# Performance work log

Measured on AMD Instinct MI355X. Metric: run time of the kernel, lower is better.

The kernel has to match this reference:

```python
import jax, jax.numpy as jnp
import numpy as np

N_S = 50000   # support points
N_Q = 50000   # query points
H = 32        # neighbors per query
K = 15        # kernel points
C_IN = 64
C_OUT = 64
G = 8         # group norm groups
RADIUS = 1.0
SIGMA = 0.6
EPS = 1e-5
NEG_SLOPE = 0.1


def setup_inputs() -> dict:
    key = jax.random.key(0)
    ks = jax.random.split(key, 8)
    s_feats = jax.random.normal(ks[0], (N_S, C_IN), jnp.float32)
    q_points = jax.random.uniform(ks[1], (N_Q, 3), jnp.float32)
    s_points = jax.random.uniform(ks[2], (N_S, 3), jnp.float32)
    # index N_S is the shadow (padding) neighbor
    neighbor_indices = jax.random.randint(ks[3], (N_Q, H), 0, N_S + 1)
    # kernel point dispositions: fixed points inside a ball of RADIUS
    d = jax.random.normal(ks[4], (K, 3), jnp.float32)
    d = d / jnp.linalg.norm(d, axis=1, keepdims=True)
    r = jax.random.uniform(ks[5], (K, 1), jnp.float32) ** (1.0 / 3.0)
    kernel_points = d * r * RADIUS                      # (K,3)
    weights = jax.random.normal(ks[6], (K, C_IN, C_OUT), jnp.float32) * (1.0 / np.sqrt(K * C_IN))
    bias = jax.random.normal(ks[7], (C_OUT,), jnp.float32) * 0.01
    gamma = jnp.ones((C_OUT,), jnp.float32)
    beta = jnp.zeros((C_OUT,), jnp.float32)
    return dict(s_feats=s_feats, q_points=q_points, s_points=s_points,
                neighbor_indices=neighbor_indices, kernel_points=kernel_points,
                weights=weights, bias=bias, gamma=gamma, beta=beta)


def kpconv(s_feats, q_points, s_points, neighbor_indices, kernel_points, weights, bias):
    # pad support set with shadow point (1e10) and zero features
    pad_pts = jnp.concatenate([s_points, jnp.full((1, 3), 1e10, s_points.dtype)], axis=0)
    pad_feats = jnp.concatenate([s_feats, jnp.zeros((1, s_feats.shape[1]), s_feats.dtype)], axis=0)
    nbr_pts = pad_pts[neighbor_indices] - q_points[:, None, :]              # (M,H,3)
    diff = nbr_pts[:, :, None, :] - kernel_points[None, None, :, :]         # (M,H,K,3)
    sq_d = jnp.sum(diff * diff, axis=-1)                                    # (M,H,K)
    # linear correlation influence, clamped at 0
    w = jnp.maximum(1.0 - jnp.sqrt(sq_d) / SIGMA, 0.0)                      # (M,H,K)
    nbr_feats = pad_feats[neighbor_indices]                                 # (M,H,Cin)
    weighted = jnp.einsum('mhk,mhc->mkc', w, nbr_feats)                     # (M,K,Cin)
    out = jnp.einsum('mkc,kcd->md', weighted, weights)                      # (M,Cout)
    # normalize by number of valid neighbors (feature-sum > 0 test, as in KPConv)
    nbr_num = jnp.sum(jnp.sum(nbr_feats, axis=-1) > 0, axis=-1)             # (M,)
    nbr_num = jnp.maximum(nbr_num, 1).astype(out.dtype)
    return out / nbr_num[:, None] + bias


def group_norm(x, gamma, beta):
    # matches GroupNorm wrapper: (M,C) -> (1,C,M) -> nn.GroupNorm -> (M,C)
    M, C = x.shape
    xg = x.T.reshape(G, C // G, M)                                          # (G,Cg,M)
    mean = xg.mean(axis=(1, 2), keepdims=True)
    var = xg.var(axis=(1, 2), keepdims=True)
    xn = ((xg - mean) / jnp.sqrt(var + EPS)).reshape(C, M).T                # (M,C)
    return xn * gamma + beta


def reference(s_feats, q_points, s_points, neighbor_indices, kernel_points, weights, bias, gamma, beta):
    x = kpconv(s_feats, q_points, s_points, neighbor_indices, kernel_points, weights, bias)
    x = group_norm(x, gamma, beta)
    x = jnp.where(x >= 0, x, NEG_SLOPE * x)                                 # LeakyReLU(0.1)
    return x[:, None, :]                                                    # unsqueeze(1): (M,1,Cout)
```

## Files before the change

kernel.cpp:

```cpp
#include <hip/hip_runtime.h>
#include <hip/hip_bf16.h>
#include <math.h>

#define NSUP 50000
#define NQ   50000
#define NH   32
#define NK   15
#define NG   8
#define INV_SIGMA (1.0f/0.6f)
#define GN_EPS 1e-5f
#define NEG  0.1f

#define QB   16
#define NBLK (NQ/QB)

#define OFF_ROWSUM 0
#define OFF_FB     50048
#define OFF_WB     (OFF_FB + 1600000)
#define OFF_PS     (OFF_WB + 30720)
#define OFF_PQ     (OFF_PS + NBLK*8)
#define OFF_STAT   (OFF_PQ + NBLK*8)

typedef __attribute__((ext_vector_type(8))) short bf16x8;
typedef __attribute__((ext_vector_type(4))) float f32x4;
typedef __attribute__((ext_vector_type(4))) unsigned int u32x4;

__device__ __forceinline__ short f2bf(float x) {
    __hip_bfloat16 h = __float2bfloat16(x);
    return *reinterpret_cast<short*>(&h);
}

__global__ __launch_bounds__(256) void k_prep(const float* __restrict__ sf,
                                              float* __restrict__ rowsum,
                                              unsigned short* __restrict__ fb,
                                              const float* __restrict__ wts,
                                              unsigned short* __restrict__ wb) {
    if (blockIdx.x < 12500) {
        int row  = (blockIdx.x * 256 + threadIdx.x) >> 6;
        int lane = threadIdx.x & 63;
        if (row >= NSUP) return;
        float v = sf[(size_t)row * 64 + lane];
        fb[(size_t)row * 64 + lane] = (unsigned short)f2bf(v);
        float s = v;
        #pragma unroll
        for (int o = 32; o; o >>= 1) s += __shfl_down(s, o);
        if (lane == 0) rowsum[row] = s;
    } else {
        int idx = (blockIdx.x - 12500) * 256 + threadIdx.x;
        if (idx >= 30 * 4 * 64 * 8) return;
        int j  = idx & 7;
        int l  = (idx >> 3) & 63;
        int n  = (idx >> 9) & 3;
        int ks = idx >> 11;
        int r  = ks * 32 + ((l >> 4) << 3) + j;
        int d  = n * 16 + (l & 15);
        wb[idx] = (unsigned short)f2bf(wts[(size_t)r * 64 + d]);
    }
}

__global__ __launch_bounds__(256, 5) void k_conv(
    const unsigned short* __restrict__ fb, const float* __restrict__ qpts,
    const float* __restrict__ spts,  const int*   __restrict__ nidx,
    const float* __restrict__ kpts,  const unsigned short* __restrict__ wb,
    const float* __restrict__ bias,  const float* __restrict__ rowsum,
    float* __restrict__ conv_out, float* __restrict__ part_s, float* __restrict__ part_q)
{
    __shared__ __align__(16) short wl16[16 * 968];
    __shared__ __align__(16) float kp4[16][4];
    __shared__ float rcl[16];

    const int tid  = threadIdx.x;
    const int wv   = tid >> 6;
    const int lane = tid & 63;
    const int g    = lane >> 4;
    const int c16  = lane & 15;

    if (tid < 16) {
        if (tid < NK) {
            kp4[tid][0] = kpts[tid*3+0];
            kp4[tid][1] = kpts[tid*3+1];
            kp4[tid][2] = kpts[tid*3+2];
        } else {
            kp4[tid][0] = 1e8f; kp4[tid][1] = 1e8f; kp4[tid][2] = 1e8f;
        }
        kp4[tid][3] = 0.f;
    }
    __syncthreads();

    const float kx = kp4[c16][0], ky = kp4[c16][1], kz = kp4[c16][2];

    const int qbase = blockIdx.x * QB;
    char*  WV  = (char*)wl16 + wv * 7424;
    float* XYP = (float*)WV;
    char*  FP  = WV + 2560;

    f32x4 pacc[4][4];
    #pragma unroll
    for (int a = 0; a < 4; a++)
        #pragma unroll
        for (int b = 0; b < 4; b++) pacc[a][b] = (f32x4){0.f,0.f,0.f,0.f};

    const int h    = lane & 31;
    const int half = lane >> 5;

    #pragma unroll
    for (int pp = 0; pp < 2; pp++) {
        const int qq = pp*2 + half;
        const int m  = qbase + wv*4 + qq;
        const float qx = qpts[m*3+0], qy = qpts[m*3+1], qz = qpts[m*3+2];
        const int  id  = nidx[(size_t)m * NH + h];
        const bool val = (id < NSUP);
        const int  ii  = val ? id : 0;
        const float dx = spts[ii*3+0]-qx, dy = spts[ii*3+1]-qy, dz = spts[ii*3+2]-qz;
        const float rs = rowsum[ii];
        unsigned long long bal = __ballot(val && rs > 0.f);
        int cA = __popcll(bal & 0xffffffffull); if (cA < 1) cA = 1;
        int cB = __popcll(bal >> 32);           if (cB < 1) cB = 1;
        if (lane == 0)  rcl[wv*4 + pp*2]     = 1.0f / (float)cA;
        if (lane == 32) rcl[wv*4 + pp*2 + 1] = 1.0f / (float)cB;
        const int si = (pp*64 + half*32 + h) * 5;
        XYP[si]     = val ? dx : 1e10f;
        XYP[si + 1] = dy;
        XYP[si + 2] = dz;
    }

    const int gr = lane >> 3;
    const int gs = lane & 7;
    int   idA[4], idB[4];
    u32x4 vA[4], vB[4];
    {
        const int m0 = qbase + wv*4;
        #pragma unroll
        for (int i = 0; i < 4; i++) idA[i] = nidx[(size_t)m0*NH + i*8 + gr];
        #pragma unroll
        for (int i = 0; i < 4; i++) {
            const int id2 = (idA[i] < NSUP) ? idA[i] : 0;
            vA[i] = *(const u32x4*)((const char*)fb + (size_t)id2*128 + gs*16);
        }
        const int m1 = qbase + wv*4 + 1;
        #pragma unroll
        for (int i = 0; i < 4; i++) idB[i] = nidx[(size_t)m1*NH + i*8 + gr];
    }

    #pragma unroll
    for (int q = 0; q < 4; q++) {
        const int pp = q >> 1, e = q & 1;
        u32x4* vc  = (q & 1) ? vB  : vA;
        u32x4* vn  = (q & 1) ? vA  : vB;
        int*   idn = (q & 1) ? idA : idB;
        int*   idt = (q & 1) ? idB : idA;

        #pragma unroll
        for (int i = 0; i < 4; i++)
            *(u32x4*)(FP + (i*8 + gr)*144 + ((gs ^ i) << 4)) = vc[i];

        if (q < 3) {
            #pragma unroll
            for (int i = 0; i < 4; i++) {
                const int id2 = (idn[i] < NSUP) ? idn[i] : 0;
                vn[i] = *(const u32x4*)((const char*)fb + (size_t)id2*128 + gs*16);
            }
        }
        if (q < 2) {
            const int mn = qbase + wv*4 + q + 2;
            #pragma unroll
            for (int i = 0; i < 4; i++) idt[i] = nidx[(size_t)mn*NH + i*8 + gr];
        }

        union { unsigned short u[8]; bf16x8 v; } ua;
        #pragma unroll
        for (int j = 0; j < 8; j++) {
            const int xi = (pp*64 + e*32 + g*8 + j) * 5;
            const float px = XYP[xi], py = XYP[xi+1], pz = XYP[xi+2];
            const float ex = px - kx, ey = py - ky, ez = pz - kz;
            const float sq = fmaf(ex, ex, fmaf(ey, ey, ez * ez));
            const float w  = fmaxf(1.0f - sqrtf(sq) * INV_SIGMA, 0.f);
            ua.u[j] = (unsigned short)f2bf(w);
        }

        #pragma unroll
        for (int ct = 0; ct < 4; ct++) {
            const char* vb = FP + (g*8)*144
                           + (((((ct << 1) | (c16 >> 3)) ^ g) & 7) << 4)
                           + ((c16 & 7) << 1);
            union { unsigned short u[8]; bf16x8 v; } ub;
            #pragma unroll
            for (int j = 0; j < 8; j++)
                ub.u[j] = *(const unsigned short*)(vb + j*144);
            pacc[q][ct] = __builtin_amdgcn_mfma_f32_16x16x32_bf16(ua.v, ub.v, pacc[q][ct], 0, 0, 0);
        }
    }

    __syncthreads();

    #pragma unroll
    for (int qq = 0; qq < 4; qq++) {
        #pragma unroll
        for (int ct = 0; ct < 4; ct++) {
            #pragma unroll
            for (int i = 0; i < 4; i++) {
                const int kk = g*4 + i;
                if (kk < NK)
                    wl16[(wv*4 + qq)*968 + kk*64 + ct*16 + c16] = f2bf(pacc[qq][ct][i]);
            }
        }
    }
    __syncthreads();

    f32x4 facc = (f32x4){0.f,0.f,0.f,0.f};
    const int z = lane >> 4;
    const short* ap = wl16 + c16*968 + z*8;
    const unsigned short* bp = wb + ((size_t)(wv * 64 + lane)) * 8;
    #pragma unroll 6
    for (int ks = 0; ks < 30; ks++) {
        bf16x8 a = *(const bf16x8*)(ap + ks*32);
        bf16x8 b = *(const bf16x8*)(bp + (size_t)ks*2048);
        facc = __builtin_amdgcn_mfma_f32_16x16x32_bf16(a, b, facc, 0, 0, 0);
    }

    const int   d  = wv*16 + c16;
    const float bs = bias[d];
    float gl = 0.f, gq = 0.f;
    #pragma unroll
    for (int i = 0; i < 4; i++) {
        const int row = z*4 + i;
        const float y = facc[i] * rcl[row] + bs;
        conv_out[(size_t)(qbase + row)*64 + d] = y;
        gl += y;
        gq = fmaf(y, y, gq);
    }
    #pragma unroll
    for (int msk = 1; msk <= 4; msk <<= 1) { gl += __shfl_xor(gl, msk); gq += __shfl_xor(gq, msk); }
    gl += __shfl_xor(gl, 16); gq += __shfl_xor(gq, 16);
    gl += __shfl_xor(gl, 32); gq += __shfl_xor(gq, 32);
    if ((lane & 55) == 0) {
        const int grp = wv*2 + (lane >> 3);
        part_s[(size_t)blockIdx.x * 8 + grp] = gl;
        part_q[(size_t)blockIdx.x * 8 + grp] = gq;
    }
}

__global__ __launch_bounds__(1024) void k_reduce(const float* __restrict__ part_s,
                                                 const float* __restrict__ part_q,
                                                 float* __restrict__ stat) {
    __shared__ double ds[128][8], dq[128][8];
    const int t = threadIdx.x;
    const int g = t & 7, chunk = t >> 3;
    const int per = (NBLK + 127) / 128;
    double s = 0.0, q = 0.0;
    int lo = chunk * per, hi = lo + per; if (hi > NBLK) hi = NBLK;
    for (int i = lo; i < hi; i++) {
        s += (double)part_s[(size_t)i * 8 + g];
        q += (double)part_q[(size_t)i * 8 + g];
    }
    ds[chunk][g] = s; dq[chunk][g] = q;
    __syncthreads();
    if (t < 8) {
        double S = 0.0, Q = 0.0;
        for (int cix = 0; cix < 128; cix++) { S += ds[cix][t]; Q += dq[cix][t]; }
        const double cnt = (double)(64 / NG) * (double)NQ;
        double mean = S / cnt;
        double var  = Q / cnt - mean * mean;
        stat[t]     = (float)mean;
        stat[8 + t] = (float)(1.0 / sqrt(var + (double)GN_EPS));
    }
}

__global__ __launch_bounds__(256) void k_apply(float* __restrict__ out,
                                               const float* __restrict__ stat,
                                               const float* __restrict__ gamma,
                                               const float* __restrict__ beta) {
    const int n4 = NQ * 64 / 4;
    for (int idx = blockIdx.x * 256 + threadIdx.x; idx < n4; idx += gridDim.x * 256) {
        float4 v = ((const float4*)out)[idx];
        const int c4 = idx & 15;
        const int g  = c4 >> 1;
        const float mean = stat[g], istd = stat[8 + g];
        const float4 ga = ((const float4*)gamma)[c4];
        const float4 be = ((const float4*)beta)[c4];
        float4 r;
        r.x = (v.x - mean) * istd * ga.x + be.x; r.x = r.x >= 0.f ? r.x : NEG * r.x;
        r.y = (v.y - mean) * istd * ga.y + be.y; r.y = r.y >= 0.f ? r.y : NEG * r.y;
        r.z = (v.z - mean) * istd * ga.z + be.z; r.z = r.z >= 0.f ? r.z : NEG * r.z;
        r.w = (v.w - mean) * istd * ga.w + be.w; r.w = r.w >= 0.f ? r.w : NEG * r.w;
        ((float4*)out)[idx] = r;
    }
}

extern "C" void kernel_launch(void* const* d_in, const int* in_sizes, int n_in,
                              void* d_out, int out_size, void* d_ws, size_t ws_size,
                              hipStream_t stream) {
    const float* sfeats = (const float*)d_in[0];
    const float* qpts   = (const float*)d_in[1];
    const float* spts   = (const float*)d_in[2];
    const int*   nidx   = (const int*)  d_in[3];
    const float* kpts   = (const float*)d_in[4];
    const float* wts    = (const float*)d_in[5];
    const float* bias   = (const float*)d_in[6];
    const float* gamma  = (const float*)d_in[7];
    const float* beta   = (const float*)d_in[8];

    float* ws = (float*)d_ws;
    float*          rowsum = ws + OFF_ROWSUM;
    unsigned short* fb     = (unsigned short*)(ws + OFF_FB);
    unsigned short* wb     = (unsigned short*)(ws + OFF_WB);
    float*          ps     = ws + OFF_PS;
    float*          pq     = ws + OFF_PQ;
    float*          stat   = ws + OFF_STAT;
    float*          out    = (float*)d_out;

    k_prep <<<dim3(12740), dim3(256), 0, stream>>>(sfeats, rowsum, fb, wts, wb);
    k_conv <<<dim3(NBLK),  dim3(256), 0, stream>>>(fb, qpts, spts, nidx, kpts,
                                                   wb, bias, rowsum, out, ps, pq);
    k_reduce<<<dim3(1),    dim3(1024), 0, stream>>>(ps, pq, stat);
    k_apply <<<dim3(1024), dim3(256), 0, stream>>>(out, stat, gamma, beta);
}
```

Measured before the change: 77.80 us.

## Split conv block across 8 waves with split-K final GEMM and perm-packed loads

Each k_conv block of 16 queries now runs 512 threads (8 waves) instead of 256. In the first phase each wave handles 2 queries instead of 4. The second GEMM is split along K across two wave halves, and the partial sums are combined through shared memory. The B-operand gather now reads 32-bit words and packs them with v_perm instead of eight 16-bit LDS loads. The XYP stride is also padded to 6 floats so it can use float2 accesses. This raises wave-level parallelism and shortens each wave's serial chain, at the cost of an extra barrier, an LDS reduction and a different occupancy/register budget.

```diff
diff --git a/kernel.cpp b/kernel.cpp
--- a/kernel.cpp
+++ b/kernel.cpp
@@ -58,19 +58,19 @@
     }
 }
 
-__global__ __launch_bounds__(256, 5) void k_conv(
+__global__ __launch_bounds__(512, 4) void k_conv(
     const unsigned short* __restrict__ fb, const float* __restrict__ qpts,
     const float* __restrict__ spts,  const int*   __restrict__ nidx,
     const float* __restrict__ kpts,  const unsigned short* __restrict__ wb,
     const float* __restrict__ bias,  const float* __restrict__ rowsum,
     float* __restrict__ conv_out, float* __restrict__ part_s, float* __restrict__ part_q)
 {
-    __shared__ __align__(16) short wl16[16 * 968];
+    __shared__ __align__(16) char U[49152];
     __shared__ __align__(16) float kp4[16][4];
     __shared__ float rcl[16];
 
     const int tid  = threadIdx.x;
-    const int wv   = tid >> 6;
+    const int w    = tid >> 6;
     const int lane = tid & 63;
     const int g    = lane >> 4;
     const int c16  = lane & 15;
@@ -90,23 +90,15 @@
     const float kx = kp4[c16][0], ky = kp4[c16][1], kz = kp4[c16][2];
 
     const int qbase = blockIdx.x * QB;
-    char*  WV  = (char*)wl16 + wv * 7424;
+    char*  WV  = U + w * 6144;
     float* XYP = (float*)WV;
-    char*  FP  = WV + 2560;
-
-    f32x4 pacc[4][4];
-    #pragma unroll
-    for (int a = 0; a < 4; a++)
-        #pragma unroll
-        for (int b = 0; b < 4; b++) pacc[a][b] = (f32x4){0.f,0.f,0.f,0.f};
+    char*  FP  = WV + 1536;
 
     const int h    = lane & 31;
     const int half = lane >> 5;
 
-    #pragma unroll
-    for (int pp = 0; pp < 2; pp++) {
-        const int qq = pp*2 + half;
-        const int m  = qbase + wv*4 + qq;
+    {
+        const int m  = qbase + w*2 + half;
         const float qx = qpts[m*3+0], qy = qpts[m*3+1], qz = qpts[m*3+2];
         const int  id  = nidx[(size_t)m * NH + h];
         const bool val = (id < NSUP);
@@ -116,11 +108,11 @@
         unsigned long long bal = __ballot(val && rs > 0.f);
         int cA = __popcll(bal & 0xffffffffull); if (cA < 1) cA = 1;
         int cB = __popcll(bal >> 32);           if (cB < 1) cB = 1;
-        if (lane == 0)  rcl[wv*4 + pp*2]     = 1.0f / (float)cA;
-        if (lane == 32) rcl[wv*4 + pp*2 + 1] = 1.0f / (float)cB;
-        const int si = (pp*64 + half*32 + h) * 5;
-        XYP[si]     = val ? dx : 1e10f;
-        XYP[si + 1] = dy;
+        if (lane == 0)  rcl[w*2]     = 1.0f / (float)cA;
+        if (lane == 32) rcl[w*2 + 1] = 1.0f / (float)cB;
+        const int si = (half*32 + h) * 6;
+        float2 xy; xy.x = val ? dx : 1e10f; xy.y = dy;
+        *(float2*)&XYP[si] = xy;
         XYP[si + 2] = dz;
     }
 
@@ -129,114 +121,128 @@
     int   idA[4], idB[4];
     u32x4 vA[4], vB[4];
     {
-        const int m0 = qbase + wv*4;
+        const int m0 = qbase + w*2;
         #pragma unroll
         for (int i = 0; i < 4; i++) idA[i] = nidx[(size_t)m0*NH + i*8 + gr];
+        #pragma unroll
+        for (int i = 0; i < 4; i++) idB[i] = nidx[(size_t)(m0+1)*NH + i*8 + gr];
         #pragma unroll
         for (int i = 0; i < 4; i++) {
             const int id2 = (idA[i] < NSUP) ? idA[i] : 0;
             vA[i] = *(const u32x4*)((const char*)fb + (size_t)id2*128 + gs*16);
         }
-        const int m1 = qbase + wv*4 + 1;
-        #pragma unroll
-        for (int i = 0; i < 4; i++) idB[i] = nidx[(size_t)m1*NH + i*8 + gr];
-    }
-
+    }
+
+    f32x4 pacc[2][4];
     #pragma unroll
-    for (int q = 0; q < 4; q++) {
-        const int pp = q >> 1, e = q & 1;
-        u32x4* vc  = (q & 1) ? vB  : vA;
-        u32x4* vn  = (q & 1) ? vA  : vB;
-        int*   idn = (q & 1) ? idA : idB;
-        int*   idt = (q & 1) ? idB : idA;
+    for (int a = 0; a < 2; a++)
+        #pragma unroll
+        for (int b = 0; b < 4; b++) pacc[a][b] = (f32x4){0.f,0.f,0.f,0.f};
+
+    const unsigned selp = 0x05040100u + ((c16 & 1) ? 0x02020202u : 0u);
+
+    #pragma unroll
+    for (int e = 0; e < 2; e++) {
+        u32x4* vc = e ? vB : vA;
 
         #pragma unroll
         for (int i = 0; i < 4; i++)
             *(u32x4*)(FP + (i*8 + gr)*144 + ((gs ^ i) << 4)) = vc[i];
 
-        if (q < 3) {
+        if (e == 0) {
             #pragma unroll
             for (int i = 0; i < 4; i++) {
-                const int id2 = (idn[i] < NSUP) ? idn[i] : 0;
-                vn[i] = *(const u32x4*)((const char*)fb + (size_t)id2*128 + gs*16);
+                const int id2 = (idB[i] < NSUP) ? idB[i] : 0;
+                vB[i] = *(const u32x4*)((const char*)fb + (size_t)id2*128 + gs*16);
             }
         }
-        if (q < 2) {
-            const int mn = qbase + wv*4 + q + 2;
+
+        union { unsigned short u[8]; bf16x8 v; } ua;
+        #pragma unroll
+        for (int j = 0; j < 8; j++) {
+            const int si = (e*32 + g*8 + j) * 6;
+            const float2 pxy = *(const float2*)&XYP[si];
+            const float  pz  = XYP[si + 2];
+            const float ex = pxy.x - kx, ey = pxy.y - ky, ez = pz - kz;
+            const float sq = fmaf(ex, ex, fmaf(ey, ey, ez * ez));
+            const float wv = fmaxf(1.0f - sqrtf(sq) * INV_SIGMA, 0.f);
+            ua.u[j] = (unsigned short)f2bf(wv);
+        }
+
+        #pragma unroll
+        for (int ct = 0; ct < 4; ct++) {
+            const char* vb = FP + g*1152
+                           + (((((ct << 1) | (c16 >> 3)) ^ g) & 7) << 4)
+                           + ((c16 & 6) << 1);
+            union { unsigned u32[4]; bf16x8 v; } ub;
             #pragma unroll
-            for (int i = 0; i < 4; i++) idt[i] = nidx[(size_t)mn*NH + i*8 + gr];
-        }
-
-        union { unsigned short u[8]; bf16x8 v; } ua;
-        #pragma unroll
-        for (int j = 0; j < 8; j++) {
-            const int xi = (pp*64 + e*32 + g*8 + j) * 5;
-            const float px = XYP[xi], py = XYP[xi+1], pz = XYP[xi+2];
-            const float ex = px - kx, ey = py - ky, ez = pz - kz;
-            const float sq = fmaf(ex, ex, fmaf(ey, ey, ez * ez));
-            const float w  = fmaxf(1.0f - sqrtf(sq) * INV_SIGMA, 0.f);
-            ua.u[j] = (unsigned short)f2bf(w);
-        }
-
-        #pragma unroll
-        for (int ct = 0; ct < 4; ct++) {
-            const char* vb = FP + (g*8)*144
-                           + (((((ct << 1) | (c16 >> 3)) ^ g) & 7) << 4)
-                           + ((c16 & 7) << 1);
-            union { unsigned short u[8]; bf16x8 v; } ub;
-            #pragma unroll
-            for (int j = 0; j < 8; j++)
-                ub.u[j] = *(const unsigned short*)(vb + j*144);
-            pacc[q][ct] = __builtin_amdgcn_mfma_f32_16x16x32_bf16(ua.v, ub.v, pacc[q][ct], 0, 0, 0);
-        }
-    }
-
-    __syncthreads();
-
+            for (int t = 0; t < 4; t++) {
+                const unsigned D0 = *(const unsigned*)(vb + t*288);
+                const unsigned D1 = *(const unsigned*)(vb + t*288 + 144);
+                ub.u32[t] = __builtin_amdgcn_perm(D1, D0, selp);
+            }
+            pacc[e][ct] = __builtin_amdgcn_mfma_f32_16x16x32_bf16(ua.v, ub.v, pacc[e][ct], 0, 0, 0);
+        }
+    }
+
+    __syncthreads();
+
+    short* wl16 = (short*)U;
     #pragma unroll
-    for (int qq = 0; qq < 4; qq++) {
+    for (int e = 0; e < 2; e++) {
         #pragma unroll
         for (int ct = 0; ct < 4; ct++) {
             #pragma unroll
             for (int i = 0; i < 4; i++) {
                 const int kk = g*4 + i;
                 if (kk < NK)
-                    wl16[(wv*4 + qq)*968 + kk*64 + ct*16 + c16] = f2bf(pacc[qq][ct][i]);
+                    wl16[(w*2 + e)*968 + kk*64 + ct*16 + c16] = f2bf(pacc[e][ct][i]);
             }
         }
     }
     __syncthreads();
 
+    const int tile = w & 3;
+    const int hf   = w >> 2;
     f32x4 facc = (f32x4){0.f,0.f,0.f,0.f};
     const int z = lane >> 4;
     const short* ap = wl16 + c16*968 + z*8;
-    const unsigned short* bp = wb + ((size_t)(wv * 64 + lane)) * 8;
-    #pragma unroll 6
-    for (int ks = 0; ks < 30; ks++) {
+    const unsigned short* bp = wb + ((size_t)(tile * 64 + lane)) * 8;
+    #pragma unroll 5
+    for (int ii = 0; ii < 15; ii++) {
+        const int ks = hf*15 + ii;
         bf16x8 a = *(const bf16x8*)(ap + ks*32);
         bf16x8 b = *(const bf16x8*)(bp + (size_t)ks*2048);
         facc = __builtin_amdgcn_mfma_f32_16x16x32_bf16(a, b, facc, 0, 0, 0);
     }
 
-    const int   d  = wv*16 + c16;
-    const float bs = bias[d];
-    float gl = 0.f, gq = 0.f;
-    #pragma unroll
-    for (int i = 0; i < 4; i++) {
-        const int row = z*4 + i;
-        const float y = facc[i] * rcl[row] + bs;
-        conv_out[(size_t)(qbase + row)*64 + d] = y;
-        gl += y;
-        gq = fmaf(y, y, gq);
-    }
-    #pragma unroll
-    for (int msk = 1; msk <= 4; msk <<= 1) { gl += __shfl_xor(gl, msk); gq += __shfl_xor(gq, msk); }
-    gl += __shfl_xor(gl, 16); gq += __shfl_xor(gq, 16);
-    gl += __shfl_xor(gl, 32); gq += __shfl_xor(gq, 32);
-    if ((lane & 55) == 0) {
-        const int grp = wv*2 + (lane >> 3);
-        part_s[(size_t)blockIdx.x * 8 + grp] = gl;
-        part_q[(size_t)blockIdx.x * 8 + grp] = gq;
+    float* P = (float*)(U + 30976);
+    if (hf == 1) *(f32x4*)(P + tile*256 + lane*4) = facc;
+    __syncthreads();
+
+    if (hf == 0) {
+        facc += *(const f32x4*)(P + tile*256 + lane*4);
+
+        const int   d  = tile*16 + c16;
+        const float bs = bias[d];
+        float gl = 0.f, gq = 0.f;
+        #pragma unroll
+        for (int i = 0; i < 4; i++) {
+            const int row = z*4 + i;
+            const float y = facc[i] * rcl[row] + bs;
+            conv_out[(size_t)(qbase + row)*64 + d] = y;
+            gl += y;
+            gq = fmaf(y, y, gq);
+        }
+        #pragma unroll
+        for (int msk = 1; msk <= 4; msk <<= 1) { gl += __shfl_xor(gl, msk); gq += __shfl_xor(gq, msk); }
+        gl += __shfl_xor(gl, 16); gq += __shfl_xor(gq, 16);
+        gl += __shfl_xor(gl, 32); gq += __shfl_xor(gq, 32);
+        if ((lane & 55) == 0) {
+            const int grp = tile*2 + (lane >> 3);
+            part_s[(size_t)blockIdx.x * 8 + grp] = gl;
+            part_q[(size_t)blockIdx.x * 8 + grp] = gq;
+        }
     }
 }
 
@@ -310,7 +316,7 @@
     float*          out    = (float*)d_out;
 
     k_prep <<<dim3(12740), dim3(256), 0, stream>>>(sfeats, rowsum, fb, wts, wb);
-    k_conv <<<dim3(NBLK),  dim3(256), 0, stream>>>(fb, qpts, spts, nidx, kpts,
+    k_conv <<<dim3(NBLK),  dim3(512), 0, stream>>>(fb, qpts, spts, nidx, kpts,
                                                    wb, bias, rowsum, out, ps, pq);
     k_reduce<<<dim3(1),    dim3(1024), 0, stream>>>(ps, pq, stat);
     k_apply <<<dim3(1024), dim3(256), 0, stream>>>(out, stat, gamma, beta);
```

After: 79.34 us. No clear change (+2.0%).

## Gather neighbor features directly into MFMA B-operand registers, skip LDS staging

Applied to the files above, without the earlier changes.

Neighbor bf16 feature rows are no longer staged through an LDS tile with 16-byte coalesced loads. Each lane now gathers its own 2-byte elements straight from global memory and packs them into the MFMA B operand with perm. Relative xyz offsets are stored as float4 so each is read with one vector LDS load. This removes the LDS write/read traffic and the swizzle arithmetic, but replaces wide coalesced gathers with 32 narrow scattered global loads per lane and a shorter prefetch distance.

```diff
diff --git a/kernel.cpp b/kernel.cpp
--- a/kernel.cpp
+++ b/kernel.cpp
@@ -23,7 +23,6 @@
 
 typedef __attribute__((ext_vector_type(8))) short bf16x8;
 typedef __attribute__((ext_vector_type(4))) float f32x4;
-typedef __attribute__((ext_vector_type(4))) unsigned int u32x4;
 
 __device__ __forceinline__ short f2bf(float x) {
     __hip_bfloat16 h = __float2bfloat16(x);
@@ -90,9 +89,7 @@
     const float kx = kp4[c16][0], ky = kp4[c16][1], kz = kp4[c16][2];
 
     const int qbase = blockIdx.x * QB;
-    char*  WV  = (char*)wl16 + wv * 7424;
-    float* XYP = (float*)WV;
-    char*  FP  = WV + 2560;
+    f32x4* XYP4 = (f32x4*)((char*)wl16 + wv * 2048);
 
     f32x4 pacc[4][4];
     #pragma unroll
@@ -118,61 +115,47 @@
         int cB = __popcll(bal >> 32);           if (cB < 1) cB = 1;
         if (lane == 0)  rcl[wv*4 + pp*2]     = 1.0f / (float)cA;
         if (lane == 32) rcl[wv*4 + pp*2 + 1] = 1.0f / (float)cB;
-        const int si = (pp*64 + half*32 + h) * 5;
-        XYP[si]     = val ? dx : 1e10f;
-        XYP[si + 1] = dy;
-        XYP[si + 2] = dz;
-    }
-
-    const int gr = lane >> 3;
-    const int gs = lane & 7;
-    int   idA[4], idB[4];
-    u32x4 vA[4], vB[4];
+        f32x4 st; st.x = val ? dx : 1e10f; st.y = dy; st.z = dz; st.w = 0.f;
+        XYP4[pp*64 + half*32 + h] = st;
+    }
+
+    int idrA[8], idrB[8];
     {
         const int m0 = qbase + wv*4;
         #pragma unroll
-        for (int i = 0; i < 4; i++) idA[i] = nidx[(size_t)m0*NH + i*8 + gr];
-        #pragma unroll
-        for (int i = 0; i < 4; i++) {
-            const int id2 = (idA[i] < NSUP) ? idA[i] : 0;
-            vA[i] = *(const u32x4*)((const char*)fb + (size_t)id2*128 + gs*16);
-        }
-        const int m1 = qbase + wv*4 + 1;
-        #pragma unroll
-        for (int i = 0; i < 4; i++) idB[i] = nidx[(size_t)m1*NH + i*8 + gr];
+        for (int j = 0; j < 8; j++) {
+            const int id = nidx[(size_t)m0*NH + g*8 + j];
+            idrA[j] = (id < NSUP) ? id : 0;
+        }
     }
 
     #pragma unroll
     for (int q = 0; q < 4; q++) {
         const int pp = q >> 1, e = q & 1;
-        u32x4* vc  = (q & 1) ? vB  : vA;
-        u32x4* vn  = (q & 1) ? vA  : vB;
-        int*   idn = (q & 1) ? idA : idB;
-        int*   idt = (q & 1) ? idB : idA;
-
-        #pragma unroll
-        for (int i = 0; i < 4; i++)
-            *(u32x4*)(FP + (i*8 + gr)*144 + ((gs ^ i) << 4)) = vc[i];
+        int* idc = (q & 1) ? idrB : idrA;
+        int* idn = (q & 1) ? idrA : idrB;
+
+        unsigned fr[32];
+        #pragma unroll
+        for (int ct = 0; ct < 4; ct++)
+            #pragma unroll
+            for (int j = 0; j < 8; j++)
+                fr[ct*8 + j] = fb[(size_t)idc[j]*64 + ct*16 + c16];
 
         if (q < 3) {
-            #pragma unroll
-            for (int i = 0; i < 4; i++) {
-                const int id2 = (idn[i] < NSUP) ? idn[i] : 0;
-                vn[i] = *(const u32x4*)((const char*)fb + (size_t)id2*128 + gs*16);
+            const int mn = qbase + wv*4 + q + 1;
+            #pragma unroll
+            for (int j = 0; j < 8; j++) {
+                const int id = nidx[(size_t)mn*NH + g*8 + j];
+                idn[j] = (id < NSUP) ? id : 0;
             }
         }
-        if (q < 2) {
-            const int mn = qbase + wv*4 + q + 2;
-            #pragma unroll
-            for (int i = 0; i < 4; i++) idt[i] = nidx[(size_t)mn*NH + i*8 + gr];
-        }
 
         union { unsigned short u[8]; bf16x8 v; } ua;
         #pragma unroll
         for (int j = 0; j < 8; j++) {
-            const int xi = (pp*64 + e*32 + g*8 + j) * 5;
-            const float px = XYP[xi], py = XYP[xi+1], pz = XYP[xi+2];
-            const float ex = px - kx, ey = py - ky, ez = pz - kz;
+            const f32x4 p = XYP4[pp*64 + e*32 + g*8 + j];
+            const float ex = p.x - kx, ey = p.y - ky, ez = p.z - kz;
             const float sq = fmaf(ex, ex, fmaf(ey, ey, ez * ez));
             const float w  = fmaxf(1.0f - sqrtf(sq) * INV_SIGMA, 0.f);
             ua.u[j] = (unsigned short)f2bf(w);
@@ -180,13 +163,10 @@
 
         #pragma unroll
         for (int ct = 0; ct < 4; ct++) {
-            const char* vb = FP + (g*8)*144
-                           + (((((ct << 1) | (c16 >> 3)) ^ g) & 7) << 4)
-                           + ((c16 & 7) << 1);
-            union { unsigned short u[8]; bf16x8 v; } ub;
-            #pragma unroll
-            for (int j = 0; j < 8; j++)
-                ub.u[j] = *(const unsigned short*)(vb + j*144);
+            union { unsigned u32[4]; bf16x8 v; } ub;
+            #pragma unroll
+            for (int t = 0; t < 4; t++)
+                ub.u32[t] = __builtin_amdgcn_perm(fr[ct*8 + 2*t + 1], fr[ct*8 + 2*t], 0x05040100u);
             pacc[q][ct] = __builtin_amdgcn_mfma_f32_16x16x32_bf16(ua.v, ub.v, pacc[q][ct], 0, 0, 0);
         }
     }
```

Measured after the change: 88.53 us. 1.14x slower.

## Fuse group-norm stat reduction into apply kernel and vectorize prep

Applied to the files above, without the earlier changes.

Removes the single-block k_reduce launch: each k_apply block now reduces the per-block partial sums itself (256 threads, unrolled double accumulators) into shared memory before normalizing. k_prep is rewritten to load float4 and store packed bf16x4, with 16 lanes per row, cutting its grid from 12740 to 3365 blocks. This saves one kernel launch and the serialized single-block reduction, but every one of the 512 apply blocks now redundantly reads all partials (about 25k floats).

```diff
diff --git a/kernel.cpp b/kernel.cpp
--- a/kernel.cpp
+++ b/kernel.cpp
@@ -19,7 +19,6 @@
 #define OFF_WB     (OFF_FB + 1600000)
 #define OFF_PS     (OFF_WB + 30720)
 #define OFF_PQ     (OFF_PS + NBLK*8)
-#define OFF_STAT   (OFF_PQ + NBLK*8)
 
 typedef __attribute__((ext_vector_type(8))) short bf16x8;
 typedef __attribute__((ext_vector_type(4))) float f32x4;
@@ -35,18 +34,21 @@
                                               unsigned short* __restrict__ fb,
                                               const float* __restrict__ wts,
                                               unsigned short* __restrict__ wb) {
-    if (blockIdx.x < 12500) {
-        int row  = (blockIdx.x * 256 + threadIdx.x) >> 6;
-        int lane = threadIdx.x & 63;
-        if (row >= NSUP) return;
-        float v = sf[(size_t)row * 64 + lane];
-        fb[(size_t)row * 64 + lane] = (unsigned short)f2bf(v);
-        float s = v;
-        #pragma unroll
-        for (int o = 32; o; o >>= 1) s += __shfl_down(s, o);
-        if (lane == 0) rowsum[row] = s;
+    if (blockIdx.x < 3125) {
+        const int lane = threadIdx.x & 63;
+        const int row  = blockIdx.x * 16 + (threadIdx.x >> 6) * 4 + (lane >> 4);
+        const int c4   = lane & 15;
+        const float4 v = ((const float4*)sf)[(size_t)row * 16 + c4];
+        ushort4 b;
+        b.x = (unsigned short)f2bf(v.x); b.y = (unsigned short)f2bf(v.y);
+        b.z = (unsigned short)f2bf(v.z); b.w = (unsigned short)f2bf(v.w);
+        *(ushort4*)&fb[(size_t)row * 64 + c4 * 4] = b;
+        float s = v.x + v.y + v.z + v.w;
+        #pragma unroll
+        for (int o = 1; o <= 8; o <<= 1) s += __shfl_xor(s, o);
+        if (c4 == 0) rowsum[row] = s;
     } else {
-        int idx = (blockIdx.x - 12500) * 256 + threadIdx.x;
+        int idx = (blockIdx.x - 3125) * 256 + threadIdx.x;
         if (idx >= 30 * 4 * 64 * 8) return;
         int j  = idx & 7;
         int l  = (idx >> 3) & 63;
@@ -240,42 +242,57 @@
     }
 }
 
-__global__ __launch_bounds__(1024) void k_reduce(const float* __restrict__ part_s,
-                                                 const float* __restrict__ part_q,
-                                                 float* __restrict__ stat) {
-    __shared__ double ds[128][8], dq[128][8];
-    const int t = threadIdx.x;
-    const int g = t & 7, chunk = t >> 3;
-    const int per = (NBLK + 127) / 128;
-    double s = 0.0, q = 0.0;
-    int lo = chunk * per, hi = lo + per; if (hi > NBLK) hi = NBLK;
-    for (int i = lo; i < hi; i++) {
-        s += (double)part_s[(size_t)i * 8 + g];
-        q += (double)part_q[(size_t)i * 8 + g];
-    }
-    ds[chunk][g] = s; dq[chunk][g] = q;
-    __syncthreads();
-    if (t < 8) {
-        double S = 0.0, Q = 0.0;
-        for (int cix = 0; cix < 128; cix++) { S += ds[cix][t]; Q += dq[cix][t]; }
-        const double cnt = (double)(64 / NG) * (double)NQ;
-        double mean = S / cnt;
-        double var  = Q / cnt - mean * mean;
-        stat[t]     = (float)mean;
-        stat[8 + t] = (float)(1.0 / sqrt(var + (double)GN_EPS));
-    }
-}
-
 __global__ __launch_bounds__(256) void k_apply(float* __restrict__ out,
-                                               const float* __restrict__ stat,
+                                               const float* __restrict__ part_s,
+                                               const float* __restrict__ part_q,
                                                const float* __restrict__ gamma,
                                                const float* __restrict__ beta) {
+    __shared__ double ds[32][8], dq[32][8];
+    __shared__ float st[16];
+    const int t = threadIdx.x;
+
+    {
+        const int gg = t & 7, chunk = t >> 3;
+        const int per = (NBLK + 31) / 32;
+        int lo = chunk * per, hi = lo + per; if (hi > NBLK) hi = NBLK;
+        double s0 = 0.0, s1 = 0.0, s2 = 0.0, s3 = 0.0;
+        double q0 = 0.0, q1 = 0.0, q2 = 0.0, q3 = 0.0;
+        int i = lo;
+        for (; i + 3 < hi; i += 4) {
+            s0 += (double)part_s[(size_t)(i+0) * 8 + gg];
+            s1 += (double)part_s[(size_t)(i+1) * 8 + gg];
+            s2 += (double)part_s[(size_t)(i+2) * 8 + gg];
+            s3 += (double)part_s[(size_t)(i+3) * 8 + gg];
+            q0 += (double)part_q[(size_t)(i+0) * 8 + gg];
+            q1 += (double)part_q[(size_t)(i+1) * 8 + gg];
+            q2 += (double)part_q[(size_t)(i+2) * 8 + gg];
+            q3 += (double)part_q[(size_t)(i+3) * 8 + gg];
+        }
+        for (; i < hi; i++) {
+            s0 += (double)part_s[(size_t)i * 8 + gg];
+            q0 += (double)part_q[(size_t)i * 8 + gg];
+        }
+        ds[chunk][gg] = (s0 + s1) + (s2 + s3);
+        dq[chunk][gg] = (q0 + q1) + (q2 + q3);
+        __syncthreads();
+        if (t < 8) {
+            double S = 0.0, Q = 0.0;
+            for (int cix = 0; cix < 32; cix++) { S += ds[cix][t]; Q += dq[cix][t]; }
+            const double cnt = (double)(64 / NG) * (double)NQ;
+            double mean = S / cnt;
+            double var  = Q / cnt - mean * mean;
+            st[t]     = (float)mean;
+            st[8 + t] = (float)(1.0 / sqrt(var + (double)GN_EPS));
+        }
+        __syncthreads();
+    }
+
     const int n4 = NQ * 64 / 4;
-    for (int idx = blockIdx.x * 256 + threadIdx.x; idx < n4; idx += gridDim.x * 256) {
+    for (int idx = blockIdx.x * 256 + t; idx < n4; idx += gridDim.x * 256) {
         float4 v = ((const float4*)out)[idx];
         const int c4 = idx & 15;
         const int g  = c4 >> 1;
-        const float mean = stat[g], istd = stat[8 + g];
+        const float mean = st[g], istd = st[8 + g];
         const float4 ga = ((const float4*)gamma)[c4];
         const float4 be = ((const float4*)beta)[c4];
         float4 r;
@@ -306,12 +323,10 @@
     unsigned short* wb     = (unsigned short*)(ws + OFF_WB);
     float*          ps     = ws + OFF_PS;
     float*          pq     = ws + OFF_PQ;
-    float*          stat   = ws + OFF_STAT;
     float*          out    = (float*)d_out;
 
-    k_prep <<<dim3(12740), dim3(256), 0, stream>>>(sfeats, rowsum, fb, wts, wb);
-    k_conv <<<dim3(NBLK),  dim3(256), 0, stream>>>(fb, qpts, spts, nidx, kpts,
-                                                   wb, bias, rowsum, out, ps, pq);
-    k_reduce<<<dim3(1),    dim3(1024), 0, stream>>>(ps, pq, stat);
-    k_apply <<<dim3(1024), dim3(256), 0, stream>>>(out, stat, gamma, beta);
-}
+    k_prep <<<dim3(3365), dim3(256), 0, stream>>>(sfeats, rowsum, fb, wts, wb);
+    k_conv <<<dim3(NBLK), dim3(256), 0, stream>>>(fb, qpts, spts, nidx, kpts,
+                                                  wb, bias, rowsum, out, ps, pq);
+    k_apply<<<dim3(512),  dim3(256), 0, stream>>>(out, ps, pq, gamma, beta);
+}
```

Result: no change. 76.78 us, median of 3 (-1.3%).
